# Kernel optimization log

Measured on AMD Instinct MI355X. Metric: run time of the kernel, lower is better.

Reference implementation:

```python
import jax, jax.numpy as jnp
import numpy as np

T, N, E, F = 20, 100000, 1600000, 3

def gru_cell(x, h, Wi, Wh, bi, bh):
    # PyTorch GRU gate order: r, z, n. x,h: [in,in] (weight rows as batch)
    gi = x @ Wi.T + bi
    gh = h @ Wh.T + bh
    ir, iz, inn = jnp.split(gi, 3, axis=1)
    hr, hz, hn = jnp.split(gh, 3, axis=1)
    r = jax.nn.sigmoid(ir + hr)
    z = jax.nn.sigmoid(iz + hz)
    n = jnp.tanh(inn + r * hn)
    return (1.0 - z) * n + z * h

def gcn_conv(x, W, edge_index, bias):
    # GCNConv_Fixed_W: add self loops, symmetric gcn_norm, aggregate src->dst
    n = x.shape[0]
    loop = jnp.arange(n, dtype=edge_index.dtype)
    src = jnp.concatenate([edge_index[0], loop])
    dst = jnp.concatenate([edge_index[1], loop])
    w = jnp.ones(src.shape[0], dtype=x.dtype)
    deg = jax.ops.segment_sum(w, dst, num_segments=n)
    dinv = jnp.where(deg > 0, jax.lax.rsqrt(deg), 0.0)
    norm = dinv[src] * w * dinv[dst]               # [E+n]
    xw = x @ W                                     # [n,F]
    msg = xw[src] * norm[:, None]                  # gather + scale
    out = jax.ops.segment_sum(msg, dst, num_segments=n)  # scatter-add
    return out + bias

def setup_inputs() -> dict:
    key = jax.random.key(0)
    ks = jax.random.split(key, 10)
    s = 0.3
    return {
        'x': jax.random.normal(ks[0], (T, N, F), jnp.float32),
        'edge_index': jax.random.randint(ks[1], (T, 2, E), 0, N, jnp.int32),
        'W0': jax.random.normal(ks[2], (F, F), jnp.float32) * s,
        'gru_Wi': jax.random.normal(ks[3], (3 * F, F), jnp.float32) * s,
        'gru_Wh': jax.random.normal(ks[4], (3 * F, F), jnp.float32) * s,
        'gru_bi': jax.random.normal(ks[5], (3 * F,), jnp.float32) * s,
        'gru_bh': jax.random.normal(ks[6], (3 * F,), jnp.float32) * s,
        'conv_bias': jnp.zeros((F,), jnp.float32),
        'lin_W': jax.random.normal(ks[7], (2, F), jnp.float32) * s,
        'lin_b': jax.random.normal(ks[8], (2,), jnp.float32) * s,
    }

def reference(x, edge_index, W0, gru_Wi, gru_Wh, gru_bi, gru_bh, conv_bias, lin_W, lin_b):
    def step(carry, inp):
        w, _ = carry
        x_t, ei_t = inp
        w_new = gru_cell(w, w, gru_Wi, gru_Wh, gru_bi, gru_bh)  # evolve weight
        h = gcn_conv(x_t, w_new, ei_t, conv_bias)               # [N,F]
        return (w_new, h), None

    h0 = jnp.zeros((x.shape[1], x.shape[2]), x.dtype)
    (w_fin, h), _ = jax.lax.scan(step, (W0, h0), (x, edge_index))
    graph_emb = jnp.mean(h, axis=0, keepdims=True)  # global mean pool, batch all-zero
    logits = graph_emb @ lin_W.T + lin_b            # [1,2]
    return logits
```

## Files before the change

kernel.cpp:

```cpp
#include <hip/hip_runtime.h>
#include <math.h>


namespace {

constexpr int T_STEPS = 20;
constexpr int N_NODES = 100000;
constexpr int E_EDGES = 1600000;

__device__ __forceinline__ float sigmoidf(float v) {
  return 1.0f / (1.0f + expf(-v));
}

__global__ void evolve_w_kernel(const float* __restrict__ W0,
                                const float* __restrict__ Wi,
                                const float* __restrict__ Wh,
                                const float* __restrict__ bi,
                                const float* __restrict__ bh,
                                float* __restrict__ wfin) {
  const int lane = threadIdx.x;
  if (lane >= 9) return;
  const int i = lane / 3, c = lane % 3;
  float wiR[3], wiZ[3], wiN[3], whR[3], whZ[3], whN[3];
#pragma unroll
  for (int k = 0; k < 3; ++k) {
    wiR[k] = Wi[(0 + c) * 3 + k];
    wiZ[k] = Wi[(3 + c) * 3 + k];
    wiN[k] = Wi[(6 + c) * 3 + k];
    whR[k] = Wh[(0 + c) * 3 + k];
    whZ[k] = Wh[(3 + c) * 3 + k];
    whN[k] = Wh[(6 + c) * 3 + k];
  }
  const float biR = bi[c], biZ = bi[3 + c], biN = bi[6 + c];
  const float bhR = bh[c], bhZ = bh[3 + c], bhN = bh[6 + c];
  float w = W0[lane];
  for (int t = 0; t < T_STEPS; ++t) {
    const float w0 = __shfl(w, 3 * i + 0, 64);
    const float w1 = __shfl(w, 3 * i + 1, 64);
    const float w2 = __shfl(w, 3 * i + 2, 64);
    const float giR = biR + w0 * wiR[0] + w1 * wiR[1] + w2 * wiR[2];
    const float giZ = biZ + w0 * wiZ[0] + w1 * wiZ[1] + w2 * wiZ[2];
    const float giN = biN + w0 * wiN[0] + w1 * wiN[1] + w2 * wiN[2];
    const float ghR = bhR + w0 * whR[0] + w1 * whR[1] + w2 * whR[2];
    const float ghZ = bhZ + w0 * whZ[0] + w1 * whZ[1] + w2 * whZ[2];
    const float ghN = bhN + w0 * whN[0] + w1 * whN[1] + w2 * whN[2];
    const float r = sigmoidf(giR + ghR);
    const float z = sigmoidf(giZ + ghZ);
    const float n = tanhf(giN + r * ghN);
    w = (1.0f - z) * n + z * w;
  }
  wfin[lane] = w;
}

__global__ __launch_bounds__(256) void degree_kernel(const int* __restrict__ dst,
                                                     int* __restrict__ deg, int E) {
  const int tid = blockIdx.x * blockDim.x + threadIdx.x;
  const int stride = gridDim.x * blockDim.x;
  const int E4 = E >> 2;
  const int4* d4 = reinterpret_cast<const int4*>(dst);
  for (int e = tid; e < E4; e += stride) {
    const int4 v = d4[e];
    atomicAdd(&deg[v.x], 1);
    atomicAdd(&deg[v.y], 1);
    atomicAdd(&deg[v.z], 1);
    atomicAdd(&deg[v.w], 1);
  }
  for (int e = (E4 << 2) + tid; e < E; e += stride) atomicAdd(&deg[dst[e]], 1);
}

__device__ __forceinline__ void block_reduce_atomic3(float a0, float a1, float a2,
                                                     double* __restrict__ gsum) {
#pragma unroll
  for (int off = 32; off > 0; off >>= 1) {
    a0 += __shfl_down(a0, off, 64);
    a1 += __shfl_down(a1, off, 64);
    a2 += __shfl_down(a2, off, 64);
  }
  __shared__ float r0[4], r1[4], r2[4];
  const int wid = threadIdx.x >> 6;
  if ((threadIdx.x & 63) == 0) { r0[wid] = a0; r1[wid] = a1; r2[wid] = a2; }
  __syncthreads();
  if (threadIdx.x == 0) {
    float t0 = 0.f, t1 = 0.f, t2 = 0.f;
    const int nw = blockDim.x >> 6;
    for (int w = 0; w < nw; ++w) { t0 += r0[w]; t1 += r1[w]; t2 += r2[w]; }
    atomicAdd(&gsum[0], (double)t0);
    atomicAdd(&gsum[1], (double)t1);
    atomicAdd(&gsum[2], (double)t2);
  }
}

__global__ __launch_bounds__(256) void node_kernel(const float* __restrict__ x,
                                                   int* __restrict__ degdinv,
                                                   const float* __restrict__ wfin,
                                                   double* __restrict__ gsum, int N) {
  __shared__ float W[9];
  if (threadIdx.x < 9) W[threadIdx.x] = wfin[threadIdx.x];
  __syncthreads();
  float a0 = 0.f, a1 = 0.f, a2 = 0.f;
  const int stride = gridDim.x * blockDim.x;
  for (int idx = blockIdx.x * blockDim.x + threadIdx.x; idx < N; idx += stride) {
    const float x0 = x[3 * idx + 0];
    const float x1 = x[3 * idx + 1];
    const float x2 = x[3 * idx + 2];
    const int dg = degdinv[idx] + 1;
    const float di = 1.0f / sqrtf((float)dg);
    degdinv[idx] = __float_as_int(di);
    const float xw0 = x0 * W[0] + x1 * W[3] + x2 * W[6];
    const float xw1 = x0 * W[1] + x1 * W[4] + x2 * W[7];
    const float xw2 = x0 * W[2] + x1 * W[5] + x2 * W[8];
    const float d2 = di * di;
    a0 += xw0 * d2; a1 += xw1 * d2; a2 += xw2 * d2;
  }
  block_reduce_atomic3(a0, a1, a2, gsum);
}

__global__ __launch_bounds__(256) void edge_kernel(const float* __restrict__ x,
                                                   const int* __restrict__ src,
                                                   const int* __restrict__ dst,
                                                   const float* __restrict__ dinv,
                                                   const float* __restrict__ wfin,
                                                   double* __restrict__ gsum, int E) {
  __shared__ float W[9];
  if (threadIdx.x < 9) W[threadIdx.x] = wfin[threadIdx.x];
  __syncthreads();
  float a0 = 0.f, a1 = 0.f, a2 = 0.f;
  const int tid = blockIdx.x * blockDim.x + threadIdx.x;
  const int stride = gridDim.x * blockDim.x;
  const int E4 = E >> 2;
  const int4* s4 = reinterpret_cast<const int4*>(src);
  const int4* d4 = reinterpret_cast<const int4*>(dst);
  for (int e = tid; e < E4; e += stride) {
    const int4 sv = s4[e];
    const int4 dv = d4[e];
    const int ss[4] = {sv.x, sv.y, sv.z, sv.w};
    const int dd[4] = {dv.x, dv.y, dv.z, dv.w};
#pragma unroll
    for (int u = 0; u < 4; ++u) {
      const int s = ss[u], d = dd[u];
      const float coef = dinv[s] * dinv[d];
      const float x0 = x[3 * s + 0];
      const float x1 = x[3 * s + 1];
      const float x2 = x[3 * s + 2];
      a0 += (x0 * W[0] + x1 * W[3] + x2 * W[6]) * coef;
      a1 += (x0 * W[1] + x1 * W[4] + x2 * W[7]) * coef;
      a2 += (x0 * W[2] + x1 * W[5] + x2 * W[8]) * coef;
    }
  }
  for (int e = (E4 << 2) + tid; e < E; e += stride) {
    const int s = src[e], d = dst[e];
    const float coef = dinv[s] * dinv[d];
    const float x0 = x[3 * s + 0];
    const float x1 = x[3 * s + 1];
    const float x2 = x[3 * s + 2];
    a0 += (x0 * W[0] + x1 * W[3] + x2 * W[6]) * coef;
    a1 += (x0 * W[1] + x1 * W[4] + x2 * W[7]) * coef;
    a2 += (x0 * W[2] + x1 * W[5] + x2 * W[8]) * coef;
  }
  block_reduce_atomic3(a0, a1, a2, gsum);
}

__global__ void final_kernel(const double* __restrict__ gsum,
                             const float* __restrict__ conv_bias,
                             const float* __restrict__ linW,
                             const float* __restrict__ linb,
                             float* __restrict__ out, int N) {
  if (threadIdx.x == 0 && blockIdx.x == 0) {
    const float e0 = (float)(gsum[0] / (double)N) + conv_bias[0];
    const float e1 = (float)(gsum[1] / (double)N) + conv_bias[1];
    const float e2 = (float)(gsum[2] / (double)N) + conv_bias[2];
    out[0] = e0 * linW[0] + e1 * linW[1] + e2 * linW[2] + linb[0];
    out[1] = e0 * linW[3] + e1 * linW[4] + e2 * linW[5] + linb[1];
  }
}

}

extern "C" void kernel_launch(void* const* d_in, const int* in_sizes, int n_in,
                              void* d_out, int out_size, void* d_ws, size_t ws_size,
                              hipStream_t stream) {
  const float* x  = (const float*)d_in[0];
  const int*   ei = (const int*)  d_in[1];
  const float* W0 = (const float*)d_in[2];
  const float* Wi = (const float*)d_in[3];
  const float* Wh = (const float*)d_in[4];
  const float* bi = (const float*)d_in[5];
  const float* bh = (const float*)d_in[6];
  const float* cb = (const float*)d_in[7];
  const float* lW = (const float*)d_in[8];
  const float* lb = (const float*)d_in[9];
  float* out = (float*)d_out;

  char* ws = (char*)d_ws;
  double* gsum  = (double*)ws;
  float*  wfin  = (float*)(ws + 64);
  int*    degdinv = (int*)(ws + 128);

  const int tlast = T_STEPS - 1;
  const float* x_last = x + (size_t)tlast * N_NODES * 3;
  const int*   src    = ei + (size_t)tlast * 2 * E_EDGES;
  const int*   dst    = src + E_EDGES;

  hipMemsetAsync(gsum, 0, 3 * sizeof(double), stream);
  hipMemsetAsync(degdinv, 0, (size_t)N_NODES * sizeof(int), stream);

  evolve_w_kernel<<<1, 64, 0, stream>>>(W0, Wi, Wh, bi, bh, wfin);
  degree_kernel<<<1024, 256, 0, stream>>>(dst, degdinv, E_EDGES);
  node_kernel<<<512, 256, 0, stream>>>(x_last, degdinv, wfin, gsum, N_NODES);
  edge_kernel<<<1024, 256, 0, stream>>>(x_last, src, dst,
                                        (const float*)degdinv, wfin, gsum, E_EDGES);
  final_kernel<<<1, 64, 0, stream>>>(gsum, cb, lW, lb, out, N_NODES);
}
```

Measured before the change: 452.1 us.

## Precompute per-node scaled xW with dinv as float4; fuse launches and final reduction

The node kernel now writes a packed float4 per node holding xW scaled by dinv plus dinv itself. The edge kernel then does one 16-byte gather for the source and one scalar gather for the destination, instead of three x loads and two dinv loads per edge. The GRU weight evolution is folded into the degree kernel, the final logits are computed by the last finishing edge block via an atomic counter, and the two memsets are merged into one. This trades an extra 1.6 MB node buffer write for fewer random gathers and fewer kernel launches.

```diff
diff --git a/kernel.cpp b/kernel.cpp
--- a/kernel.cpp
+++ b/kernel.cpp
@@ -4,56 +4,53 @@
 
 namespace {
 
-constexpr int T_STEPS = 20;
-constexpr int N_NODES = 100000;
-constexpr int E_EDGES = 1600000;
+constexpr int T_STEPS  = 20;
+constexpr int N_NODES  = 100000;
+constexpr int E_EDGES  = 1600000;
+constexpr int EDGE_BLOCKS = 1024;
 
 __device__ __forceinline__ float sigmoidf(float v) {
   return 1.0f / (1.0f + expf(-v));
 }
 
-__global__ void evolve_w_kernel(const float* __restrict__ W0,
-                                const float* __restrict__ Wi,
-                                const float* __restrict__ Wh,
-                                const float* __restrict__ bi,
-                                const float* __restrict__ bh,
-                                float* __restrict__ wfin) {
-  const int lane = threadIdx.x;
-  if (lane >= 9) return;
-  const int i = lane / 3, c = lane % 3;
-  float wiR[3], wiZ[3], wiN[3], whR[3], whZ[3], whN[3];
+__global__ __launch_bounds__(256) void degree_evolve_kernel(
+    const int* __restrict__ dst, int* __restrict__ deg, int E,
+    const float* __restrict__ W0, const float* __restrict__ Wi,
+    const float* __restrict__ Wh, const float* __restrict__ bi,
+    const float* __restrict__ bh, float* __restrict__ wfin) {
+  if (blockIdx.x == 0 && threadIdx.x < 9) {
+    const int lane = threadIdx.x;
+    const int i = lane / 3, c = lane % 3;
+    float wiR[3], wiZ[3], wiN[3], whR[3], whZ[3], whN[3];
 #pragma unroll
-  for (int k = 0; k < 3; ++k) {
-    wiR[k] = Wi[(0 + c) * 3 + k];
-    wiZ[k] = Wi[(3 + c) * 3 + k];
-    wiN[k] = Wi[(6 + c) * 3 + k];
-    whR[k] = Wh[(0 + c) * 3 + k];
-    whZ[k] = Wh[(3 + c) * 3 + k];
-    whN[k] = Wh[(6 + c) * 3 + k];
-  }
-  const float biR = bi[c], biZ = bi[3 + c], biN = bi[6 + c];
-  const float bhR = bh[c], bhZ = bh[3 + c], bhN = bh[6 + c];
-  float w = W0[lane];
-  for (int t = 0; t < T_STEPS; ++t) {
-    const float w0 = __shfl(w, 3 * i + 0, 64);
-    const float w1 = __shfl(w, 3 * i + 1, 64);
-    const float w2 = __shfl(w, 3 * i + 2, 64);
-    const float giR = biR + w0 * wiR[0] + w1 * wiR[1] + w2 * wiR[2];
-    const float giZ = biZ + w0 * wiZ[0] + w1 * wiZ[1] + w2 * wiZ[2];
-    const float giN = biN + w0 * wiN[0] + w1 * wiN[1] + w2 * wiN[2];
-    const float ghR = bhR + w0 * whR[0] + w1 * whR[1] + w2 * whR[2];
-    const float ghZ = bhZ + w0 * whZ[0] + w1 * whZ[1] + w2 * whZ[2];
-    const float ghN = bhN + w0 * whN[0] + w1 * whN[1] + w2 * whN[2];
-    const float r = sigmoidf(giR + ghR);
-    const float z = sigmoidf(giZ + ghZ);
-    const float n = tanhf(giN + r * ghN);
-    w = (1.0f - z) * n + z * w;
-  }
-  wfin[lane] = w;
-}
-
-__global__ __launch_bounds__(256) void degree_kernel(const int* __restrict__ dst,
-                                                     int* __restrict__ deg, int E) {
+    for (int k = 0; k < 3; ++k) {
+      wiR[k] = Wi[(0 + c) * 3 + k];
+      wiZ[k] = Wi[(3 + c) * 3 + k];
+      wiN[k] = Wi[(6 + c) * 3 + k];
+      whR[k] = Wh[(0 + c) * 3 + k];
+      whZ[k] = Wh[(3 + c) * 3 + k];
+      whN[k] = Wh[(6 + c) * 3 + k];
+    }
+    const float biR = bi[c], biZ = bi[3 + c], biN = bi[6 + c];
+    const float bhR = bh[c], bhZ = bh[3 + c], bhN = bh[6 + c];
+    float w = W0[lane];
+    for (int t = 0; t < T_STEPS; ++t) {
+      const float w0 = __shfl(w, 3 * i + 0, 64);
+      const float w1 = __shfl(w, 3 * i + 1, 64);
+      const float w2 = __shfl(w, 3 * i + 2, 64);
+      const float giR = biR + w0 * wiR[0] + w1 * wiR[1] + w2 * wiR[2];
+      const float giZ = biZ + w0 * wiZ[0] + w1 * wiZ[1] + w2 * wiZ[2];
+      const float giN = biN + w0 * wiN[0] + w1 * wiN[1] + w2 * wiN[2];
+      const float ghR = bhR + w0 * whR[0] + w1 * whR[1] + w2 * whR[2];
+      const float ghZ = bhZ + w0 * whZ[0] + w1 * whZ[1] + w2 * whZ[2];
+      const float ghN = bhN + w0 * whN[0] + w1 * whN[1] + w2 * whN[2];
+      const float r = sigmoidf(giR + ghR);
+      const float z = sigmoidf(giZ + ghZ);
+      const float n = tanhf(giN + r * ghN);
+      w = (1.0f - z) * n + z * w;
+    }
+    wfin[lane] = w;
+  }
   const int tid = blockIdx.x * blockDim.x + threadIdx.x;
   const int stride = gridDim.x * blockDim.x;
   const int E4 = E >> 2;
@@ -68,8 +65,7 @@
   for (int e = (E4 << 2) + tid; e < E; e += stride) atomicAdd(&deg[dst[e]], 1);
 }
 
-__device__ __forceinline__ void block_reduce_atomic3(float a0, float a1, float a2,
-                                                     double* __restrict__ gsum) {
+__device__ __forceinline__ void block_reduce3(float& a0, float& a1, float& a2) {
 #pragma unroll
   for (int off = 32; off > 0; off >>= 1) {
     a0 += __shfl_down(a0, off, 64);
@@ -81,17 +77,15 @@
   if ((threadIdx.x & 63) == 0) { r0[wid] = a0; r1[wid] = a1; r2[wid] = a2; }
   __syncthreads();
   if (threadIdx.x == 0) {
-    float t0 = 0.f, t1 = 0.f, t2 = 0.f;
+    a0 = a1 = a2 = 0.f;
     const int nw = blockDim.x >> 6;
-    for (int w = 0; w < nw; ++w) { t0 += r0[w]; t1 += r1[w]; t2 += r2[w]; }
-    atomicAdd(&gsum[0], (double)t0);
-    atomicAdd(&gsum[1], (double)t1);
-    atomicAdd(&gsum[2], (double)t2);
+    for (int w = 0; w < nw; ++w) { a0 += r0[w]; a1 += r1[w]; a2 += r2[w]; }
   }
 }
 
 __global__ __launch_bounds__(256) void node_kernel(const float* __restrict__ x,
-                                                   int* __restrict__ degdinv,
+                                                   const int* __restrict__ deg,
+                                                   float4* __restrict__ v4,
                                                    const float* __restrict__ wfin,
                                                    double* __restrict__ gsum, int N) {
   __shared__ float W[9];
@@ -103,27 +97,29 @@
     const float x0 = x[3 * idx + 0];
     const float x1 = x[3 * idx + 1];
     const float x2 = x[3 * idx + 2];
-    const int dg = degdinv[idx] + 1;
+    const int dg = deg[idx] + 1;
     const float di = 1.0f / sqrtf((float)dg);
-    degdinv[idx] = __float_as_int(di);
-    const float xw0 = x0 * W[0] + x1 * W[3] + x2 * W[6];
-    const float xw1 = x0 * W[1] + x1 * W[4] + x2 * W[7];
-    const float xw2 = x0 * W[2] + x1 * W[5] + x2 * W[8];
-    const float d2 = di * di;
-    a0 += xw0 * d2; a1 += xw1 * d2; a2 += xw2 * d2;
-  }
-  block_reduce_atomic3(a0, a1, a2, gsum);
-}
-
-__global__ __launch_bounds__(256) void edge_kernel(const float* __restrict__ x,
-                                                   const int* __restrict__ src,
-                                                   const int* __restrict__ dst,
-                                                   const float* __restrict__ dinv,
-                                                   const float* __restrict__ wfin,
-                                                   double* __restrict__ gsum, int E) {
-  __shared__ float W[9];
-  if (threadIdx.x < 9) W[threadIdx.x] = wfin[threadIdx.x];
-  __syncthreads();
+    const float s0 = (x0 * W[0] + x1 * W[3] + x2 * W[6]) * di;
+    const float s1 = (x0 * W[1] + x1 * W[4] + x2 * W[7]) * di;
+    const float s2 = (x0 * W[2] + x1 * W[5] + x2 * W[8]) * di;
+    v4[idx] = make_float4(s0, s1, s2, di);
+    a0 += s0 * di; a1 += s1 * di; a2 += s2 * di;
+  }
+  block_reduce3(a0, a1, a2);
+  if (threadIdx.x == 0) {
+    atomicAdd(&gsum[0], (double)a0);
+    atomicAdd(&gsum[1], (double)a1);
+    atomicAdd(&gsum[2], (double)a2);
+  }
+}
+
+__global__ __launch_bounds__(256) void edge_final_kernel(
+    const int* __restrict__ src, const int* __restrict__ dst,
+    const float4* __restrict__ v4, double* __restrict__ gsum,
+    unsigned* __restrict__ counter,
+    const float* __restrict__ conv_bias, const float* __restrict__ linW,
+    const float* __restrict__ linb, float* __restrict__ out, int E, int N) {
+  const float* vw = reinterpret_cast<const float*>(v4);
   float a0 = 0.f, a1 = 0.f, a2 = 0.f;
   const int tid = blockIdx.x * blockDim.x + threadIdx.x;
   const int stride = gridDim.x * blockDim.x;
@@ -133,44 +129,44 @@
   for (int e = tid; e < E4; e += stride) {
     const int4 sv = s4[e];
     const int4 dv = d4[e];
-    const int ss[4] = {sv.x, sv.y, sv.z, sv.w};
-    const int dd[4] = {dv.x, dv.y, dv.z, dv.w};
-#pragma unroll
-    for (int u = 0; u < 4; ++u) {
-      const int s = ss[u], d = dd[u];
-      const float coef = dinv[s] * dinv[d];
-      const float x0 = x[3 * s + 0];
-      const float x1 = x[3 * s + 1];
-      const float x2 = x[3 * s + 2];
-      a0 += (x0 * W[0] + x1 * W[3] + x2 * W[6]) * coef;
-      a1 += (x0 * W[1] + x1 * W[4] + x2 * W[7]) * coef;
-      a2 += (x0 * W[2] + x1 * W[5] + x2 * W[8]) * coef;
+    {
+      const float4 a = v4[sv.x]; const float b = vw[4 * dv.x + 3];
+      a0 += a.x * b; a1 += a.y * b; a2 += a.z * b;
+    }
+    {
+      const float4 a = v4[sv.y]; const float b = vw[4 * dv.y + 3];
+      a0 += a.x * b; a1 += a.y * b; a2 += a.z * b;
+    }
+    {
+      const float4 a = v4[sv.z]; const float b = vw[4 * dv.z + 3];
+      a0 += a.x * b; a1 += a.y * b; a2 += a.z * b;
+    }
+    {
+      const float4 a = v4[sv.w]; const float b = vw[4 * dv.w + 3];
+      a0 += a.x * b; a1 += a.y * b; a2 += a.z * b;
     }
   }
   for (int e = (E4 << 2) + tid; e < E; e += stride) {
-    const int s = src[e], d = dst[e];
-    const float coef = dinv[s] * dinv[d];
-    const float x0 = x[3 * s + 0];
-    const float x1 = x[3 * s + 1];
-    const float x2 = x[3 * s + 2];
-    a0 += (x0 * W[0] + x1 * W[3] + x2 * W[6]) * coef;
-    a1 += (x0 * W[1] + x1 * W[4] + x2 * W[7]) * coef;
-    a2 += (x0 * W[2] + x1 * W[5] + x2 * W[8]) * coef;
-  }
-  block_reduce_atomic3(a0, a1, a2, gsum);
-}
-
-__global__ void final_kernel(const double* __restrict__ gsum,
-                             const float* __restrict__ conv_bias,
-                             const float* __restrict__ linW,
-                             const float* __restrict__ linb,
-                             float* __restrict__ out, int N) {
-  if (threadIdx.x == 0 && blockIdx.x == 0) {
-    const float e0 = (float)(gsum[0] / (double)N) + conv_bias[0];
-    const float e1 = (float)(gsum[1] / (double)N) + conv_bias[1];
-    const float e2 = (float)(gsum[2] / (double)N) + conv_bias[2];
-    out[0] = e0 * linW[0] + e1 * linW[1] + e2 * linW[2] + linb[0];
-    out[1] = e0 * linW[3] + e1 * linW[4] + e2 * linW[5] + linb[1];
+    const float4 a = v4[src[e]]; const float b = vw[4 * dst[e] + 3];
+    a0 += a.x * b; a1 += a.y * b; a2 += a.z * b;
+  }
+  block_reduce3(a0, a1, a2);
+  if (threadIdx.x == 0) {
+    atomicAdd(&gsum[0], (double)a0);
+    atomicAdd(&gsum[1], (double)a1);
+    atomicAdd(&gsum[2], (double)a2);
+    __threadfence();
+    const unsigned done = atomicAdd(counter, 1u);
+    if (done == gridDim.x - 1) {
+      const double g0 = atomicAdd(&gsum[0], 0.0);
+      const double g1 = atomicAdd(&gsum[1], 0.0);
+      const double g2 = atomicAdd(&gsum[2], 0.0);
+      const float e0 = (float)(g0 / (double)N) + conv_bias[0];
+      const float e1 = (float)(g1 / (double)N) + conv_bias[1];
+      const float e2 = (float)(g2 / (double)N) + conv_bias[2];
+      out[0] = e0 * linW[0] + e1 * linW[1] + e2 * linW[2] + linb[0];
+      out[1] = e0 * linW[3] + e1 * linW[4] + e2 * linW[5] + linb[1];
+    }
   }
 }
 
@@ -192,22 +188,23 @@
   float* out = (float*)d_out;
 
   char* ws = (char*)d_ws;
-  double* gsum  = (double*)ws;
-  float*  wfin  = (float*)(ws + 64);
-  int*    degdinv = (int*)(ws + 128);
+  double*   gsum    = (double*)ws;
+  unsigned* counter = (unsigned*)(ws + 64);
+  int*      deg     = (int*)(ws + 128);
+  float*    wfin    = (float*)(ws + 400128);
+  float4*   v4      = (float4*)(ws + 400192);
 
   const int tlast = T_STEPS - 1;
   const float* x_last = x + (size_t)tlast * N_NODES * 3;
   const int*   src    = ei + (size_t)tlast * 2 * E_EDGES;
   const int*   dst    = src + E_EDGES;
 
-  hipMemsetAsync(gsum, 0, 3 * sizeof(double), stream);
-  hipMemsetAsync(degdinv, 0, (size_t)N_NODES * sizeof(int), stream);
-
-  evolve_w_kernel<<<1, 64, 0, stream>>>(W0, Wi, Wh, bi, bh, wfin);
-  degree_kernel<<<1024, 256, 0, stream>>>(dst, degdinv, E_EDGES);
-  node_kernel<<<512, 256, 0, stream>>>(x_last, degdinv, wfin, gsum, N_NODES);
-  edge_kernel<<<1024, 256, 0, stream>>>(x_last, src, dst,
-                                        (const float*)degdinv, wfin, gsum, E_EDGES);
-  final_kernel<<<1, 64, 0, stream>>>(gsum, cb, lW, lb, out, N_NODES);
-}
+  hipMemsetAsync(ws, 0, 400128, stream);
+
+  degree_evolve_kernel<<<1024, 256, 0, stream>>>(dst, deg, E_EDGES,
+                                                 W0, Wi, Wh, bi, bh, wfin);
+  node_kernel<<<512, 256, 0, stream>>>(x_last, deg, v4, wfin, gsum, N_NODES);
+  edge_final_kernel<<<EDGE_BLOCKS, 256, 0, stream>>>(src, dst, v4, gsum, counter,
+                                                     cb, lW, lb, out,
+                                                     E_EDGES, N_NODES);
+}
```

Measured after the change: 445.6 us. No clear change (-1.4%).
